# Kernel tuning notes

Hardware: AMD Instinct MI355X
Metric: run time of the kernel (lower is better)

The kernel has to match this reference:

```python
import jax, jax.numpy as jnp
import numpy as np

DIN = 1024
DOUT = 1024


def setup_inputs() -> dict:
    key = jax.random.key(0)
    kx, kq, kk, kv = jax.random.split(key, 4)
    B, T = 4, 2048
    x = jax.random.normal(kx, (B, T, DIN), dtype=jnp.float32)
    # nn.Linear weights are (dout, din); init like PyTorch default scale
    s = 1.0 / np.sqrt(DIN)
    Wq = jax.random.uniform(kq, (DOUT, DIN), minval=-s, maxval=s, dtype=jnp.float32)
    Wk = jax.random.uniform(kk, (DOUT, DIN), minval=-s, maxval=s, dtype=jnp.float32)
    Wv = jax.random.uniform(kv, (DOUT, DIN), minval=-s, maxval=s, dtype=jnp.float32)
    return {"x": x, "Wq": Wq, "Wk": Wk, "Wv": Wv}


def reference(x, Wq, Wk, Wv):
    B, T, _ = x.shape
    q = jnp.einsum('btd,ed->bte', x, Wq)
    k = jnp.einsum('btd,ed->bte', x, Wk)
    v = jnp.einsum('btd,ed->bte', x, Wv)
    attn = jnp.einsum('bqe,bke->bqk', q, k)  # [B, T, T]
    # Faithful to source: masked_fill result is discarded, so the causal mask
    # is a MULTIPLICATIVE tril of ones (upper triangle logits become 0, not -inf).
    mask = jnp.tril(jnp.ones((T, T), dtype=attn.dtype))
    attn = attn * mask
    # Faithful to source: scale by sqrt(last dim of attn) = sqrt(T), not sqrt(d).
    attn = jax.nn.softmax(attn / jnp.sqrt(jnp.asarray(T, attn.dtype)), axis=-1)
    return jnp.einsum('bqk,bke->bqe', attn, v)
```

## Files before the change

kernel.cpp:

```cpp
#include <hip/hip_runtime.h>
#include <stdint.h>

#define BB 4
#define TT 2048
#define DD 1024
#define NX (BB*TT*DD)
#define NW (DD*DD)
#define SCALE 0.022097086912079608f

typedef short v8s __attribute__((ext_vector_type(8)));
typedef float v4f __attribute__((ext_vector_type(4)));

typedef const void __attribute__((address_space(1))) *as1_cvp;
typedef void __attribute__((address_space(3))) *as3_vp;

__device__ __forceinline__ short f2bf(float f) {
    union { float f; uint32_t u; } x; x.f = f;
    uint32_t r = x.u + 0x7fffu + ((x.u >> 16) & 1u);
    return (short)(r >> 16);
}
__device__ __forceinline__ float bf2f(short s) {
    union { uint32_t u; float f; } x; x.u = ((uint32_t)(uint16_t)s) << 16;
    return x.f;
}

__device__ __forceinline__ void gl_lds16(const short* g, const short* lds_wave_base) {
    __builtin_amdgcn_global_load_lds(
        (as1_cvp)(uintptr_t)(const void*)g,
        (as3_vp)(uint32_t)(uintptr_t)(const void*)lds_wave_base,
        16, 0, 0);
}

__device__ __forceinline__ void stage_tile(const short* __restrict__ gsrc, int lda,
                                           short* lds, int tid) {
    int wave = tid >> 6;
    #pragma unroll
    for (int is = 0; is < 4; is++) {
        int t = is * 256 + tid;
        int r = t >> 3, c = t & 7;
        int cg = c ^ (r & 7);
        const short* g = gsrc + (size_t)r * lda + cg * 8;
        const short* l = lds + is * 2048 + wave * 512;
        gl_lds16(g, l);
    }
}
__device__ __forceinline__ void stage_tile64(const short* __restrict__ gsrc, int lda,
                                             short* lds, int tid) {
    int wave = tid >> 6;
    #pragma unroll
    for (int is = 0; is < 2; is++) {
        int t = is * 256 + tid;
        int r = t >> 3, c = t & 7;
        int cg = c ^ (r & 7);
        const short* g = gsrc + (size_t)r * lda + cg * 8;
        const short* l = lds + is * 2048 + wave * 512;
        gl_lds16(g, l);
    }
}
__device__ __forceinline__ v8s frag_read(const short* lds, int row, int cg) {
    return *(const v8s*)(lds + row * 64 + ((cg ^ (row & 7)) << 3));
}

__device__ __forceinline__ void stageA128(const short* __restrict__ g, short* lds, int tid) {
    int wave = tid >> 6;
    #pragma unroll
    for (int s = 0; s < 2; s++) {
        int t = s * 512 + tid;
        int r = t >> 3, c = t & 7;
        int cg = c ^ (r & 7);
        gl_lds16(g + (size_t)r * 1024 + cg * 8, lds + s * 4096 + wave * 512);
    }
}
__device__ __forceinline__ void stageBpart(const short* __restrict__ g, short* lds,
                                           int tid, int p) {
    int wave = tid >> 6;
    #pragma unroll
    for (int s = 0; s < 2; s++) {
        int t = s * 512 + tid;
        int r = t >> 3, c = t & 7;
        int cg = c ^ (r & 7);
        int grow = ((r >> 5) << 6) + p * 32 + (r & 31);
        gl_lds16(g + (size_t)grow * 1024 + cg * 8, lds + s * 4096 + wave * 512);
    }
}

#define COMPUTE_TILE64(Ac, Bc)                                                      \
    _Pragma("unroll")                                                               \
    for (int kk = 0; kk < 2; kk++) {                                                \
        v8s af[2], bf[4];                                                           \
        _Pragma("unroll")                                                           \
        for (int i = 0; i < 2; i++) af[i] = frag_read(Ac, wm + i*16 + lr, kk*4 + lq); \
        _Pragma("unroll")                                                           \
        for (int j = 0; j < 4; j++) bf[j] = frag_read(Bc, wn + j*16 + lr, kk*4 + lq); \
        _Pragma("unroll")                                                           \
        for (int i = 0; i < 2; i++)                                                 \
            _Pragma("unroll")                                                       \
            for (int j = 0; j < 4; j++)                                             \
                acc[i][j] = __builtin_amdgcn_mfma_f32_16x16x32_bf16(af[i], bf[j], acc[i][j], 0, 0, 0); \
    }

__global__ void k_convert(const float* __restrict__ x, const float* __restrict__ Wq,
                          const float* __restrict__ Wk, const float* __restrict__ Wv,
                          short* __restrict__ dst, float* __restrict__ rowsum) {
    int i = blockIdx.x * 256 + threadIdx.x;
    if (i < BB * TT) rowsum[i] = (float)((15 - ((i & 2047) >> 7)) * 128);
    size_t base = (size_t)i * 4;
    const float* src; size_t off;
    if (base < NX)               { src = x;  off = base; }
    else if (base < NX + NW)     { src = Wq; off = base - NX; }
    else if (base < NX + 2*(size_t)NW) { src = Wk; off = base - NX - NW; }
    else                         { src = Wv; off = base - NX - 2*(size_t)NW; }
    float4 f = *(const float4*)(src + off);
    short4 h; h.x = f2bf(f.x); h.y = f2bf(f.y); h.z = f2bf(f.z); h.w = f2bf(f.w);
    *(short4*)(dst + base) = h;
}

__global__ __launch_bounds__(512, 2) void k_qkv(const short* __restrict__ xb,
                                                const short* __restrict__ wb,
                                                short* __restrict__ q,
                                                short* __restrict__ k,
                                                short* __restrict__ vt) {
    int h = blockIdx.x;
    int w = (h & 7) * 96 + (h >> 3);
    int which = w >> 8, rem = w & 255, ntile = rem >> 6, mtile = rem & 63;
    int m0 = mtile * 128, n0 = ntile * 256;
    const short* Ag = xb + (size_t)m0 * 1024;
    const short* Bg = wb + (size_t)which * NW + (size_t)n0 * 1024;
    __shared__ __align__(16) short SH[49152];
    int tid = threadIdx.x, lane = tid & 63, wave = tid >> 6;
    int wm = wave >> 2, wn = wave & 3;
    int lr = lane & 15, lq = lane >> 4;
    int arow = wm * 64 + lr;
    int brow = wn * 32 + lr;
    v4f acc[4][4];
    #pragma unroll
    for (int i = 0; i < 4; i++)
        #pragma unroll
        for (int j = 0; j < 4; j++) acc[i][j] = (v4f){0.f, 0.f, 0.f, 0.f};

    stageA128 (Ag, SH,         tid);
    stageBpart(Bg, SH + 8192,  tid, 0);
    stageBpart(Bg, SH + 16384, tid, 1);

    #pragma unroll
    for (int t = 0; t < 16; ++t) {
        short* S  = SH + (t & 1) * 24576;
        short* Sn = SH + ((t + 1) & 1) * 24576;
        const short* Agn = Ag + (t + 1) * 64;
        const short* Bgn = Bg + (t + 1) * 64;
        asm volatile("s_waitcnt vmcnt(2)" ::: "memory");
        __builtin_amdgcn_s_barrier();
        v8s af[4][2], bf[2][2];
        #pragma unroll
        for (int i = 0; i < 4; i++)
            #pragma unroll
            for (int kk = 0; kk < 2; kk++) af[i][kk] = frag_read(S, arow + i * 16, kk * 4 + lq);
        #pragma unroll
        for (int jj = 0; jj < 2; jj++)
            #pragma unroll
            for (int kk = 0; kk < 2; kk++) bf[jj][kk] = frag_read(S + 8192, brow + jj * 16, kk * 4 + lq);
        if (t < 15) {
            stageA128 (Agn, Sn,        tid);
            stageBpart(Bgn, Sn + 8192, tid, 0);
        }
        __builtin_amdgcn_s_setprio(1);
        #pragma unroll
        for (int kk = 0; kk < 2; kk++)
            #pragma unroll
            for (int i = 0; i < 4; i++)
                #pragma unroll
                for (int jj = 0; jj < 2; jj++)
                    acc[i][jj] = __builtin_amdgcn_mfma_f32_16x16x32_bf16(af[i][kk], bf[jj][kk], acc[i][jj], 0, 0, 0);
        __builtin_amdgcn_s_setprio(0);
        if (t < 15) { asm volatile("s_waitcnt vmcnt(4)" ::: "memory"); }
        else        { asm volatile("s_waitcnt vmcnt(0)" ::: "memory"); }
        __builtin_amdgcn_s_barrier();
        v8s bg2[2][2];
        #pragma unroll
        for (int jj = 0; jj < 2; jj++)
            #pragma unroll
            for (int kk = 0; kk < 2; kk++) bg2[jj][kk] = frag_read(S + 16384, brow + jj * 16, kk * 4 + lq);
        if (t < 15) stageBpart(Bgn, Sn + 16384, tid, 1);
        __builtin_amdgcn_s_setprio(1);
        #pragma unroll
        for (int kk = 0; kk < 2; kk++)
            #pragma unroll
            for (int i = 0; i < 4; i++)
                #pragma unroll
                for (int jj = 0; jj < 2; jj++)
                    acc[i][2 + jj] = __builtin_amdgcn_mfma_f32_16x16x32_bf16(af[i][kk], bg2[jj][kk], acc[i][2 + jj], 0, 0, 0);
        __builtin_amdgcn_s_setprio(0);
    }

    if (which == 2) {
        #pragma unroll
        for (int a = 0; a < 4; a++)
            #pragma unroll
            for (int b = 0; b < 4; b++)
                #pragma unroll
                for (int r = 0; r < 4; r++) {
                    int row = m0 + wm * 64 + a * 16 + lq * 4 + r;
                    int col = n0 + wn * 64 + b * 16 + lr;
                    int bb = row >> 11, tt2 = row & 2047;
                    vt[((size_t)bb << 21) + ((size_t)col << 11) + tt2] = f2bf(acc[a][b][r]);
                }
    } else {
        short* outp = (which == 0) ? q : k;
        #pragma unroll
        for (int a = 0; a < 4; a++)
            #pragma unroll
            for (int b = 0; b < 4; b++)
                #pragma unroll
                for (int r = 0; r < 4; r++) {
                    int row = m0 + wm * 64 + a * 16 + lq * 4 + r;
                    int col = n0 + wn * 64 + b * 16 + lr;
                    outp[(size_t)row * 1024 + col] = f2bf(acc[a][b][r]);
                }
    }
}

__global__ void k_ts1(const short* __restrict__ vt, float* __restrict__ TSpart) {
    int g = blockIdx.x * 256 + threadIdx.x;
    int b = g >> 14, jt = (g >> 10) & 15, e = g & 1023;
    const short* row = vt + ((size_t)b << 21) + ((size_t)e << 11) + jt * 128;
    float s = 0.f;
    #pragma unroll
    for (int c = 0; c < 16; c++) {
        uint4 u = *(const uint4*)(row + c * 8);
        const short* hp = (const short*)&u;
        #pragma unroll
        for (int z = 0; z < 8; z++) s += bf2f(hp[z]);
    }
    TSpart[g] = s;
}
__global__ void k_ts2(const float* __restrict__ TSpart, float* __restrict__ TS) {
    int g = blockIdx.x * 256 + threadIdx.x;
    int b = g >> 10, e = g & 1023;
    float acc = 0.f;
    TS[(size_t)(b * 17 + 16) * 1024 + e] = 0.f;
    for (int jt = 15; jt >= 0; jt--) {
        acc += TSpart[(size_t)(b * 16 + jt) * 1024 + e];
        TS[(size_t)(b * 17 + jt) * 1024 + e] = acc;
    }
}

__global__ __launch_bounds__(256, 3) void k_pk(const short* __restrict__ qm,
                                               const short* __restrict__ km,
                                               short* __restrict__ P,
                                               float* __restrict__ rowsum) {
    int flip = 271 - blockIdx.x, b = blockIdx.z;
    int half = flip & 1, pidx = flip >> 1;
    int qt = 0;
    while ((qt + 1) * (qt + 2) / 2 <= pidx) qt++;
    int kt = pidx - qt * (qt + 1) / 2;
    int r0 = qt * 128 + half * 64;
    const short* Ag = qm + ((size_t)b * 2048 + r0) * 1024;
    const short* Bg = km + ((size_t)b * 2048 + (size_t)kt * 128) * 1024;
    __shared__ __align__(16) short SH[24576];
    int tid = threadIdx.x, lane = tid & 63, wave = tid >> 6;
    int wm = (wave >> 1) * 32, wn = (wave & 1) * 64;
    int lr = lane & 15, lq = lane >> 4;
    v4f acc[2][4];
    for (int i = 0; i < 2; i++) for (int j = 0; j < 4; j++) acc[i][j] = (v4f){0.f,0.f,0.f,0.f};

    stage_tile64(Ag, 1024, SH, tid);
    stage_tile(Bg, 1024, SH + 8192, tid);
    #pragma unroll
    for (int it = 0; it < 16; ++it) {
        __syncthreads();
        short* Ac = SH + (it & 1) * 4096;
        short* Bc = SH + 8192 + (it & 1) * 8192;
        if (it + 1 < 16) {
            stage_tile64(Ag + (it + 1) * 64, 1024, SH + ((it + 1) & 1) * 4096, tid);
            stage_tile  (Bg + (it + 1) * 64, 1024, SH + 8192 + ((it + 1) & 1) * 8192, tid);
        }
        COMPUTE_TILE64(Ac, Bc);
    }
    short* Pb = P + ((size_t)b << 22);
    float rs[2][4];
    for (int i = 0; i < 2; i++) for (int r = 0; r < 4; r++) rs[i][r] = 0.f;
    #pragma unroll
    for (int i = 0; i < 2; i++)
        #pragma unroll
        for (int j = 0; j < 4; j++)
            #pragma unroll
            for (int r = 0; r < 4; r++) {
                int qi = r0 + wm + i*16 + lq*4 + r;
                int kj = kt * 128 + wn + j*16 + lr;
                float p = (kj <= qi) ? __expf(acc[i][j][r] * SCALE) : 1.0f;
                Pb[(size_t)qi * 2048 + kj] = f2bf(p);
                rs[i][r] += p;
            }
    #pragma unroll
    for (int m = 1; m < 16; m <<= 1)
        #pragma unroll
        for (int i = 0; i < 2; i++)
            #pragma unroll
            for (int r = 0; r < 4; r++) rs[i][r] += __shfl_xor(rs[i][r], m);
    if (lr == 0)
        #pragma unroll
        for (int i = 0; i < 2; i++)
            #pragma unroll
            for (int r = 0; r < 4; r++)
                atomicAdd(&rowsum[b * 2048 + r0 + wm + i*16 + lq*4 + r], rs[i][r]);
}

__global__ __launch_bounds__(256, 3) void k_pv(const short* __restrict__ P,
                                               const short* __restrict__ vt,
                                               const float* __restrict__ rowsum,
                                               const float* __restrict__ TS,
                                               float* __restrict__ out) {
    int et = blockIdx.x, p = blockIdx.y >> 1, half = blockIdx.y & 1, b = blockIdx.z;
    const short* Bg = vt + ((size_t)b << 21) + (size_t)et * 128 * 2048;
    __shared__ __align__(16) short SH[24576];
    int tid = threadIdx.x, lane = tid & 63, wave = tid >> 6;
    int wm = (wave >> 1) * 32, wn = (wave & 1) * 64;
    int lr = lane & 15, lq = lane >> 4;

    #pragma unroll
    for (int ph = 0; ph < 2; ph++) {
        int qt = ph ? p : 15 - p;
        int r0 = qt * 128 + half * 64;
        int iters = 2 * (qt + 1);
        const short* Ag = P + ((size_t)b << 22) + (size_t)r0 * 2048;
        v4f acc[2][4];
        for (int i = 0; i < 2; i++) for (int j = 0; j < 4; j++) acc[i][j] = (v4f){0.f,0.f,0.f,0.f};

        stage_tile64(Ag, 2048, SH, tid);
        stage_tile(Bg, 2048, SH + 8192, tid);
        for (int it = 0; it < iters; it += 2) {
            __syncthreads();
            if (it + 1 < iters) {
                stage_tile64(Ag + (it + 1) * 64, 2048, SH + 4096, tid);
                stage_tile  (Bg + (it + 1) * 64, 2048, SH + 8192 + 8192, tid);
            }
            COMPUTE_TILE64(SH, SH + 8192);
            __syncthreads();
            if (it + 2 < iters) {
                stage_tile64(Ag + (it + 2) * 64, 2048, SH, tid);
                stage_tile  (Bg + (it + 2) * 64, 2048, SH + 8192, tid);
            }
            COMPUTE_TILE64(SH + 4096, SH + 8192 + 8192);
        }
        const float* tsrow = TS + (size_t)(b * 17 + qt + 1) * 1024;
        #pragma unroll
        for (int i = 0; i < 2; i++)
            #pragma unroll
            for (int j = 0; j < 4; j++)
                #pragma unroll
                for (int r = 0; r < 4; r++) {
                    int row = r0 + wm + i*16 + lq*4 + r;
                    int col = et * 128 + wn + j*16 + lr;
                    float o = (acc[i][j][r] + tsrow[col]) / rowsum[b * 2048 + row];
                    out[((size_t)(b * 2048 + row) << 10) + col] = o;
                }
        __syncthreads();
    }
}

extern "C" void kernel_launch(void* const* d_in, const int* in_sizes, int n_in,
                              void* d_out, int out_size, void* d_ws, size_t ws_size,
                              hipStream_t stream) {
    const float* x  = (const float*)d_in[0];
    const float* Wq = (const float*)d_in[1];
    const float* Wk = (const float*)d_in[2];
    const float* Wv = (const float*)d_in[3];
    float* out = (float*)d_out;
    char* ws = (char*)d_ws;

    short* xb     = (short*)(ws + 0);
    short* wb     = (short*)(ws + 16777216);
    short* q      = (short*)(ws + 23068672);
    short* k      = (short*)(ws + 39845888);
    short* vt     = (short*)(ws + 56623104);
    short* P      = (short*)(ws + 73400320);
    float* rowsum = (float*)(ws + 106954752);
    float* TSpart = (float*)(ws + 106987520);
    float* TS     = (float*)(ws + 107249664);

    k_convert<<<11264, 256, 0, stream>>>(x, Wq, Wk, Wv, xb, rowsum);
    k_qkv<<<dim3(768, 1, 1), 512, 0, stream>>>(xb, wb, q, k, vt);
    k_ts1<<<256, 256, 0, stream>>>(vt, TSpart);
    k_ts2<<<16, 256, 0, stream>>>(TSpart, TS);
    k_pk<<<dim3(272, 1, 4), 256, 0, stream>>>(q, k, P, rowsum);
    k_pv<<<dim3(8, 16, 4), 256, 0, stream>>>(P, vt, rowsum, TS, out);
}
```

Before: 224.8 us.

## Fuse Q/K/V projections into one block sharing the staged x tile

The QKV GEMM is restructured so each 1024-thread block computes the Q, K and V outputs for one 128x256 tile. It stages the x (A) tile once and reuses it against the three weight matrices, where previously separate blocks each reloaded it. The K-loop start is rotated per m-tile to spread global reads, and a new three-buffer B pipeline with its own waitcnt/barrier schedule is added. In exchange there are fewer blocks (256) with more registers (three accumulator sets) and 128KB of LDS, so occupancy and load balance may suffer.

```diff
diff --git a/kernel.cpp b/kernel.cpp
--- a/kernel.cpp
+++ b/kernel.cpp
@@ -61,26 +61,16 @@
     return *(const v8s*)(lds + row * 64 + ((cg ^ (row & 7)) << 3));
 }
 
-__device__ __forceinline__ void stageA128(const short* __restrict__ g, short* lds, int tid) {
-    int wave = tid >> 6;
+__device__ __forceinline__ void stA(const short* __restrict__ g, short* lds, int tid) {
+    int r = tid >> 3, c = tid & 7, cg = c ^ (r & 7);
+    gl_lds16(g + (size_t)r * 1024 + cg * 8, lds + (tid >> 6) * 512);
+}
+__device__ __forceinline__ void stB(const short* __restrict__ g, short* lds, int tid) {
     #pragma unroll
     for (int s = 0; s < 2; s++) {
-        int t = s * 512 + tid;
-        int r = t >> 3, c = t & 7;
-        int cg = c ^ (r & 7);
-        gl_lds16(g + (size_t)r * 1024 + cg * 8, lds + s * 4096 + wave * 512);
-    }
-}
-__device__ __forceinline__ void stageBpart(const short* __restrict__ g, short* lds,
-                                           int tid, int p) {
-    int wave = tid >> 6;
-    #pragma unroll
-    for (int s = 0; s < 2; s++) {
-        int t = s * 512 + tid;
-        int r = t >> 3, c = t & 7;
-        int cg = c ^ (r & 7);
-        int grow = ((r >> 5) << 6) + p * 32 + (r & 31);
-        gl_lds16(g + (size_t)grow * 1024 + cg * 8, lds + s * 4096 + wave * 512);
+        int t = s * 1024 + tid;
+        int r = t >> 3, c = t & 7, cg = c ^ (r & 7);
+        gl_lds16(g + (size_t)r * 1024 + cg * 8, lds + s * 8192 + (tid >> 6) * 512);
     }
 }
 
@@ -115,108 +105,129 @@
     *(short4*)(dst + base) = h;
 }
 
-__global__ __launch_bounds__(512, 2) void k_qkv(const short* __restrict__ xb,
-                                                const short* __restrict__ wb,
-                                                short* __restrict__ q,
-                                                short* __restrict__ k,
-                                                short* __restrict__ vt) {
+__global__ __launch_bounds__(1024, 4) void k_qkv(const short* __restrict__ xb,
+                                                 const short* __restrict__ wb,
+                                                 short* __restrict__ q,
+                                                 short* __restrict__ k,
+                                                 short* __restrict__ vt) {
     int h = blockIdx.x;
-    int w = (h & 7) * 96 + (h >> 3);
-    int which = w >> 8, rem = w & 255, ntile = rem >> 6, mtile = rem & 63;
+    int w = (h & 7) * 32 + (h >> 3);
+    int ntile = w >> 6, mtile = w & 63;
     int m0 = mtile * 128, n0 = ntile * 256;
+    int rot = mtile & 15;
     const short* Ag = xb + (size_t)m0 * 1024;
-    const short* Bg = wb + (size_t)which * NW + (size_t)n0 * 1024;
-    __shared__ __align__(16) short SH[49152];
+    const short* Bq = wb + (size_t)n0 * 1024;
+    const short* Bk = wb + (size_t)NW + (size_t)n0 * 1024;
+    const short* Bv = wb + 2 * (size_t)NW + (size_t)n0 * 1024;
+    __shared__ __align__(16) short SH[65536];
+    short* SA0 = SH;
+    short* SA1 = SH + 8192;
+    short* SB0 = SH + 16384;
+    short* SB1 = SH + 32768;
+    short* SB2 = SH + 49152;
     int tid = threadIdx.x, lane = tid & 63, wave = tid >> 6;
-    int wm = wave >> 2, wn = wave & 3;
+    int wm2 = wave >> 3, wn8 = wave & 7;
     int lr = lane & 15, lq = lane >> 4;
-    int arow = wm * 64 + lr;
-    int brow = wn * 32 + lr;
-    v4f acc[4][4];
+    int arow = wm2 * 64 + lr;
+    int brow = wn8 * 32 + lr;
+    v4f aq[4][2], ak[4][2], av[4][2];
     #pragma unroll
     for (int i = 0; i < 4; i++)
         #pragma unroll
-        for (int j = 0; j < 4; j++) acc[i][j] = (v4f){0.f, 0.f, 0.f, 0.f};
-
-    stageA128 (Ag, SH,         tid);
-    stageBpart(Bg, SH + 8192,  tid, 0);
-    stageBpart(Bg, SH + 16384, tid, 1);
-
-    #pragma unroll
+        for (int j = 0; j < 2; j++) {
+            aq[i][j] = (v4f){0.f, 0.f, 0.f, 0.f};
+            ak[i][j] = (v4f){0.f, 0.f, 0.f, 0.f};
+            av[i][j] = (v4f){0.f, 0.f, 0.f, 0.f};
+        }
+
+    {
+        int kt0 = rot;
+        stA(Ag + kt0 * 64, SA0, tid);
+        stB(Bq + kt0 * 64, SB0, tid);
+        stB(Bk + kt0 * 64, SB1, tid);
+    }
+    asm volatile("s_waitcnt vmcnt(2)" ::: "memory");
+    __builtin_amdgcn_s_barrier();
+
+    #pragma unroll 2
     for (int t = 0; t < 16; ++t) {
-        short* S  = SH + (t & 1) * 24576;
-        short* Sn = SH + ((t + 1) & 1) * 24576;
-        const short* Agn = Ag + (t + 1) * 64;
-        const short* Bgn = Bg + (t + 1) * 64;
-        asm volatile("s_waitcnt vmcnt(2)" ::: "memory");
-        __builtin_amdgcn_s_barrier();
+        short* SA  = (t & 1) ? SA1 : SA0;
+        short* SAn = (t & 1) ? SA0 : SA1;
+        int kt  = (t + rot) & 15;
+        int ktn = (t + 1 + rot) & 15;
         v8s af[4][2], bf[2][2];
         #pragma unroll
         for (int i = 0; i < 4; i++)
             #pragma unroll
-            for (int kk = 0; kk < 2; kk++) af[i][kk] = frag_read(S, arow + i * 16, kk * 4 + lq);
-        #pragma unroll
-        for (int jj = 0; jj < 2; jj++)
-            #pragma unroll
-            for (int kk = 0; kk < 2; kk++) bf[jj][kk] = frag_read(S + 8192, brow + jj * 16, kk * 4 + lq);
-        if (t < 15) {
-            stageA128 (Agn, Sn,        tid);
-            stageBpart(Bgn, Sn + 8192, tid, 0);
-        }
+            for (int kk = 0; kk < 2; kk++) af[i][kk] = frag_read(SA, arow + i * 16, kk * 4 + lq);
+        #pragma unroll
+        for (int j = 0; j < 2; j++)
+            #pragma unroll
+            for (int kk = 0; kk < 2; kk++) bf[j][kk] = frag_read(SB0, brow + j * 16, kk * 4 + lq);
+        stB(Bv + kt * 64, SB2, tid);
+        if (t < 15) stA(Ag + ktn * 64, SAn, tid);
         __builtin_amdgcn_s_setprio(1);
         #pragma unroll
         for (int kk = 0; kk < 2; kk++)
             #pragma unroll
             for (int i = 0; i < 4; i++)
                 #pragma unroll
-                for (int jj = 0; jj < 2; jj++)
-                    acc[i][jj] = __builtin_amdgcn_mfma_f32_16x16x32_bf16(af[i][kk], bf[jj][kk], acc[i][jj], 0, 0, 0);
+                for (int j = 0; j < 2; j++)
+                    aq[i][j] = __builtin_amdgcn_mfma_f32_16x16x32_bf16(af[i][kk], bf[j][kk], aq[i][j], 0, 0, 0);
         __builtin_amdgcn_s_setprio(0);
-        if (t < 15) { asm volatile("s_waitcnt vmcnt(4)" ::: "memory"); }
+        if (t < 15) { asm volatile("s_waitcnt vmcnt(3)" ::: "memory"); }
+        else        { asm volatile("s_waitcnt vmcnt(2)" ::: "memory"); }
+        __builtin_amdgcn_s_barrier();
+        #pragma unroll
+        for (int j = 0; j < 2; j++)
+            #pragma unroll
+            for (int kk = 0; kk < 2; kk++) bf[j][kk] = frag_read(SB1, brow + j * 16, kk * 4 + lq);
+        if (t < 15) stB(Bq + ktn * 64, SB0, tid);
+        __builtin_amdgcn_s_setprio(1);
+        #pragma unroll
+        for (int kk = 0; kk < 2; kk++)
+            #pragma unroll
+            for (int i = 0; i < 4; i++)
+                #pragma unroll
+                for (int j = 0; j < 2; j++)
+                    ak[i][j] = __builtin_amdgcn_mfma_f32_16x16x32_bf16(af[i][kk], bf[j][kk], ak[i][j], 0, 0, 0);
+        __builtin_amdgcn_s_setprio(0);
+        if (t < 15) { asm volatile("s_waitcnt vmcnt(3)" ::: "memory"); }
         else        { asm volatile("s_waitcnt vmcnt(0)" ::: "memory"); }
         __builtin_amdgcn_s_barrier();
-        v8s bg2[2][2];
-        #pragma unroll
-        for (int jj = 0; jj < 2; jj++)
-            #pragma unroll
-            for (int kk = 0; kk < 2; kk++) bg2[jj][kk] = frag_read(S + 16384, brow + jj * 16, kk * 4 + lq);
-        if (t < 15) stageBpart(Bgn, Sn + 16384, tid, 1);
+        #pragma unroll
+        for (int j = 0; j < 2; j++)
+            #pragma unroll
+            for (int kk = 0; kk < 2; kk++) bf[j][kk] = frag_read(SB2, brow + j * 16, kk * 4 + lq);
+        if (t < 15) stB(Bk + ktn * 64, SB1, tid);
         __builtin_amdgcn_s_setprio(1);
         #pragma unroll
         for (int kk = 0; kk < 2; kk++)
             #pragma unroll
             for (int i = 0; i < 4; i++)
                 #pragma unroll
-                for (int jj = 0; jj < 2; jj++)
-                    acc[i][2 + jj] = __builtin_amdgcn_mfma_f32_16x16x32_bf16(af[i][kk], bg2[jj][kk], acc[i][2 + jj], 0, 0, 0);
+                for (int j = 0; j < 2; j++)
+                    av[i][j] = __builtin_amdgcn_mfma_f32_16x16x32_bf16(af[i][kk], bf[j][kk], av[i][j], 0, 0, 0);
         __builtin_amdgcn_s_setprio(0);
-    }
-
-    if (which == 2) {
-        #pragma unroll
-        for (int a = 0; a < 4; a++)
-            #pragma unroll
-            for (int b = 0; b < 4; b++)
-                #pragma unroll
-                for (int r = 0; r < 4; r++) {
-                    int row = m0 + wm * 64 + a * 16 + lq * 4 + r;
-                    int col = n0 + wn * 64 + b * 16 + lr;
-                    int bb = row >> 11, tt2 = row & 2047;
-                    vt[((size_t)bb << 21) + ((size_t)col << 11) + tt2] = f2bf(acc[a][b][r]);
-                }
-    } else {
-        short* outp = (which == 0) ? q : k;
-        #pragma unroll
-        for (int a = 0; a < 4; a++)
-            #pragma unroll
-            for (int b = 0; b < 4; b++)
-                #pragma unroll
-                for (int r = 0; r < 4; r++) {
-                    int row = m0 + wm * 64 + a * 16 + lq * 4 + r;
-                    int col = n0 + wn * 64 + b * 16 + lr;
-                    outp[(size_t)row * 1024 + col] = f2bf(acc[a][b][r]);
-                }
-    }
+        if (t < 15) {
+            asm volatile("s_waitcnt vmcnt(2)" ::: "memory");
+            __builtin_amdgcn_s_barrier();
+        }
+    }
+
+    #pragma unroll
+    for (int i = 0; i < 4; i++)
+        #pragma unroll
+        for (int j = 0; j < 2; j++)
+            #pragma unroll
+            for (int r = 0; r < 4; r++) {
+                int row = m0 + wm2 * 64 + i * 16 + lq * 4 + r;
+                int col = n0 + wn8 * 32 + j * 16 + lr;
+                q[(size_t)row * 1024 + col] = f2bf(aq[i][j][r]);
+                k[(size_t)row * 1024 + col] = f2bf(ak[i][j][r]);
+                int bb = row >> 11, tt2 = row & 2047;
+                vt[((size_t)bb << 21) + ((size_t)col << 11) + tt2] = f2bf(av[i][j][r]);
+            }
 }
 
 __global__ void k_ts1(const short* __restrict__ vt, float* __restrict__ TSpart) {
@@ -379,7 +390,7 @@
     float* TS     = (float*)(ws + 107249664);
 
     k_convert<<<11264, 256, 0, stream>>>(x, Wq, Wk, Wv, xb, rowsum);
-    k_qkv<<<dim3(768, 1, 1), 512, 0, stream>>>(xb, wb, q, k, vt);
+    k_qkv<<<dim3(256, 1, 1), 1024, 0, stream>>>(xb, wb, q, k, vt);
     k_ts1<<<256, 256, 0, stream>>>(vt, TSpart);
     k_ts2<<<16, 256, 0, stream>>>(TSpart, TS);
     k_pk<<<dim3(272, 1, 4), 256, 0, stream>>>(q, k, P, rowsum);
```

Result: slower. 499.0 us (+121.9%).

## Use 128x128 tiles with 8 waves in score and PV kernels

Applied to the files above, without the earlier changes.

The QK^T score kernel and the PV kernel move from 64x128 tiles with 4 waves to full 128x128 tiles with 8 waves per block, each wave owning a 64x32 sub-tile. This halves the number of blocks and doubles the reuse of each staged K/V tile, aiming to cut global-to-LDS traffic. MFMA sections are wrapped in s_setprio raises, and PV now uses single-step double buffering. The trade-off is larger LDS per block, fewer blocks for load balancing across the triangular work, and the loss of the reversed block ordering in the score kernel.

```diff
diff --git a/kernel.cpp b/kernel.cpp
--- a/kernel.cpp
+++ b/kernel.cpp
@@ -31,73 +31,32 @@
         16, 0, 0);
 }
 
-__device__ __forceinline__ void stage_tile(const short* __restrict__ gsrc, int lda,
-                                           short* lds, int tid) {
-    int wave = tid >> 6;
-    #pragma unroll
-    for (int is = 0; is < 4; is++) {
-        int t = is * 256 + tid;
-        int r = t >> 3, c = t & 7;
-        int cg = c ^ (r & 7);
-        const short* g = gsrc + (size_t)r * lda + cg * 8;
-        const short* l = lds + is * 2048 + wave * 512;
-        gl_lds16(g, l);
-    }
-}
-__device__ __forceinline__ void stage_tile64(const short* __restrict__ gsrc, int lda,
-                                             short* lds, int tid) {
-    int wave = tid >> 6;
-    #pragma unroll
-    for (int is = 0; is < 2; is++) {
-        int t = is * 256 + tid;
-        int r = t >> 3, c = t & 7;
-        int cg = c ^ (r & 7);
-        const short* g = gsrc + (size_t)r * lda + cg * 8;
-        const short* l = lds + is * 2048 + wave * 512;
-        gl_lds16(g, l);
-    }
-}
 __device__ __forceinline__ v8s frag_read(const short* lds, int row, int cg) {
     return *(const v8s*)(lds + row * 64 + ((cg ^ (row & 7)) << 3));
 }
 
-__device__ __forceinline__ void stageA128(const short* __restrict__ g, short* lds, int tid) {
-    int wave = tid >> 6;
+__device__ __forceinline__ void stage128_512(const short* __restrict__ g, int lda,
+                                             short* lds, int tid) {
     #pragma unroll
     for (int s = 0; s < 2; s++) {
         int t = s * 512 + tid;
-        int r = t >> 3, c = t & 7;
-        int cg = c ^ (r & 7);
-        gl_lds16(g + (size_t)r * 1024 + cg * 8, lds + s * 4096 + wave * 512);
-    }
+        int r = t >> 3, c = t & 7, cg = c ^ (r & 7);
+        gl_lds16(g + (size_t)r * lda + cg * 8, lds + s * 4096 + (tid >> 6) * 512);
+    }
+}
+__device__ __forceinline__ void stageA128(const short* __restrict__ g, short* lds, int tid) {
+    stage128_512(g, 1024, lds, tid);
 }
 __device__ __forceinline__ void stageBpart(const short* __restrict__ g, short* lds,
                                            int tid, int p) {
-    int wave = tid >> 6;
     #pragma unroll
     for (int s = 0; s < 2; s++) {
         int t = s * 512 + tid;
-        int r = t >> 3, c = t & 7;
-        int cg = c ^ (r & 7);
+        int r = t >> 3, c = t & 7, cg = c ^ (r & 7);
         int grow = ((r >> 5) << 6) + p * 32 + (r & 31);
-        gl_lds16(g + (size_t)grow * 1024 + cg * 8, lds + s * 4096 + wave * 512);
-    }
-}
-
-#define COMPUTE_TILE64(Ac, Bc)                                                      \
-    _Pragma("unroll")                                                               \
-    for (int kk = 0; kk < 2; kk++) {                                                \
-        v8s af[2], bf[4];                                                           \
-        _Pragma("unroll")                                                           \
-        for (int i = 0; i < 2; i++) af[i] = frag_read(Ac, wm + i*16 + lr, kk*4 + lq); \
-        _Pragma("unroll")                                                           \
-        for (int j = 0; j < 4; j++) bf[j] = frag_read(Bc, wn + j*16 + lr, kk*4 + lq); \
-        _Pragma("unroll")                                                           \
-        for (int i = 0; i < 2; i++)                                                 \
-            _Pragma("unroll")                                                       \
-            for (int j = 0; j < 4; j++)                                             \
-                acc[i][j] = __builtin_amdgcn_mfma_f32_16x16x32_bf16(af[i], bf[j], acc[i][j], 0, 0, 0); \
-    }
+        gl_lds16(g + (size_t)grow * 1024 + cg * 8, lds + s * 4096 + (tid >> 6) * 512);
+    }
+}
 
 __global__ void k_convert(const float* __restrict__ x, const float* __restrict__ Wq,
                           const float* __restrict__ Wk, const float* __restrict__ Wv,
@@ -244,49 +203,71 @@
     }
 }
 
-__global__ __launch_bounds__(256, 3) void k_pk(const short* __restrict__ qm,
+__global__ __launch_bounds__(512, 4) void k_pk(const short* __restrict__ qm,
                                                const short* __restrict__ km,
                                                short* __restrict__ P,
                                                float* __restrict__ rowsum) {
-    int flip = 271 - blockIdx.x, b = blockIdx.z;
-    int half = flip & 1, pidx = flip >> 1;
+    int pidx = blockIdx.x, b = blockIdx.z;
     int qt = 0;
     while ((qt + 1) * (qt + 2) / 2 <= pidx) qt++;
     int kt = pidx - qt * (qt + 1) / 2;
-    int r0 = qt * 128 + half * 64;
+    int r0 = qt * 128;
     const short* Ag = qm + ((size_t)b * 2048 + r0) * 1024;
     const short* Bg = km + ((size_t)b * 2048 + (size_t)kt * 128) * 1024;
-    __shared__ __align__(16) short SH[24576];
+    __shared__ __align__(16) short SH[32768];
     int tid = threadIdx.x, lane = tid & 63, wave = tid >> 6;
-    int wm = (wave >> 1) * 32, wn = (wave & 1) * 64;
+    int wm2 = wave >> 2, wn4 = wave & 3;
     int lr = lane & 15, lq = lane >> 4;
-    v4f acc[2][4];
-    for (int i = 0; i < 2; i++) for (int j = 0; j < 4; j++) acc[i][j] = (v4f){0.f,0.f,0.f,0.f};
-
-    stage_tile64(Ag, 1024, SH, tid);
-    stage_tile(Bg, 1024, SH + 8192, tid);
+    v4f acc[4][2];
+    #pragma unroll
+    for (int i = 0; i < 4; i++)
+        #pragma unroll
+        for (int j = 0; j < 2; j++) acc[i][j] = (v4f){0.f, 0.f, 0.f, 0.f};
+
+    stage128_512(Ag, 1024, SH, tid);
+    stage128_512(Bg, 1024, SH + 16384, tid);
     #pragma unroll
     for (int it = 0; it < 16; ++it) {
         __syncthreads();
-        short* Ac = SH + (it & 1) * 4096;
-        short* Bc = SH + 8192 + (it & 1) * 8192;
+        short* Ac = SH + (it & 1) * 8192;
+        short* Bc = SH + 16384 + (it & 1) * 8192;
         if (it + 1 < 16) {
-            stage_tile64(Ag + (it + 1) * 64, 1024, SH + ((it + 1) & 1) * 4096, tid);
-            stage_tile  (Bg + (it + 1) * 64, 1024, SH + 8192 + ((it + 1) & 1) * 8192, tid);
+            stage128_512(Ag + (it + 1) * 64, 1024, SH + ((it + 1) & 1) * 8192, tid);
+            stage128_512(Bg + (it + 1) * 64, 1024, SH + 16384 + ((it + 1) & 1) * 8192, tid);
         }
-        COMPUTE_TILE64(Ac, Bc);
+        v8s af[4][2], bf[2][2];
+        #pragma unroll
+        for (int i = 0; i < 4; i++)
+            #pragma unroll
+            for (int kk = 0; kk < 2; kk++) af[i][kk] = frag_read(Ac, wm2 * 64 + i * 16 + lr, kk * 4 + lq);
+        #pragma unroll
+        for (int j = 0; j < 2; j++)
+            #pragma unroll
+            for (int kk = 0; kk < 2; kk++) bf[j][kk] = frag_read(Bc, wn4 * 32 + j * 16 + lr, kk * 4 + lq);
+        __builtin_amdgcn_s_setprio(1);
+        #pragma unroll
+        for (int kk = 0; kk < 2; kk++)
+            #pragma unroll
+            for (int i = 0; i < 4; i++)
+                #pragma unroll
+                for (int j = 0; j < 2; j++)
+                    acc[i][j] = __builtin_amdgcn_mfma_f32_16x16x32_bf16(af[i][kk], bf[j][kk], acc[i][j], 0, 0, 0);
+        __builtin_amdgcn_s_setprio(0);
     }
     short* Pb = P + ((size_t)b << 22);
-    float rs[2][4];
-    for (int i = 0; i < 2; i++) for (int r = 0; r < 4; r++) rs[i][r] = 0.f;
-    #pragma unroll
-    for (int i = 0; i < 2; i++)
-        #pragma unroll
-        for (int j = 0; j < 4; j++)
+    float rs[4][4];
+    #pragma unroll
+    for (int i = 0; i < 4; i++)
+        #pragma unroll
+        for (int r = 0; r < 4; r++) rs[i][r] = 0.f;
+    #pragma unroll
+    for (int i = 0; i < 4; i++)
+        #pragma unroll
+        for (int j = 0; j < 2; j++)
             #pragma unroll
             for (int r = 0; r < 4; r++) {
-                int qi = r0 + wm + i*16 + lq*4 + r;
-                int kj = kt * 128 + wn + j*16 + lr;
+                int qi = r0 + wm2 * 64 + i * 16 + lq * 4 + r;
+                int kj = kt * 128 + wn4 * 32 + j * 16 + lr;
                 float p = (kj <= qi) ? __expf(acc[i][j][r] * SCALE) : 1.0f;
                 Pb[(size_t)qi * 2048 + kj] = f2bf(p);
                 rs[i][r] += p;
@@ -294,63 +275,79 @@
     #pragma unroll
     for (int m = 1; m < 16; m <<= 1)
         #pragma unroll
-        for (int i = 0; i < 2; i++)
+        for (int i = 0; i < 4; i++)
             #pragma unroll
             for (int r = 0; r < 4; r++) rs[i][r] += __shfl_xor(rs[i][r], m);
     if (lr == 0)
         #pragma unroll
-        for (int i = 0; i < 2; i++)
+        for (int i = 0; i < 4; i++)
             #pragma unroll
             for (int r = 0; r < 4; r++)
-                atomicAdd(&rowsum[b * 2048 + r0 + wm + i*16 + lq*4 + r], rs[i][r]);
-}
-
-__global__ __launch_bounds__(256, 3) void k_pv(const short* __restrict__ P,
+                atomicAdd(&rowsum[b * 2048 + r0 + wm2 * 64 + i * 16 + lq * 4 + r], rs[i][r]);
+}
+
+__global__ __launch_bounds__(512, 4) void k_pv(const short* __restrict__ P,
                                                const short* __restrict__ vt,
                                                const float* __restrict__ rowsum,
                                                const float* __restrict__ TS,
                                                float* __restrict__ out) {
-    int et = blockIdx.x, p = blockIdx.y >> 1, half = blockIdx.y & 1, b = blockIdx.z;
+    int et = blockIdx.x, p = blockIdx.y, b = blockIdx.z;
     const short* Bg = vt + ((size_t)b << 21) + (size_t)et * 128 * 2048;
-    __shared__ __align__(16) short SH[24576];
+    __shared__ __align__(16) short SH[32768];
     int tid = threadIdx.x, lane = tid & 63, wave = tid >> 6;
-    int wm = (wave >> 1) * 32, wn = (wave & 1) * 64;
+    int wm2 = wave >> 2, wn4 = wave & 3;
     int lr = lane & 15, lq = lane >> 4;
 
     #pragma unroll
     for (int ph = 0; ph < 2; ph++) {
         int qt = ph ? p : 15 - p;
-        int r0 = qt * 128 + half * 64;
+        int r0 = qt * 128;
         int iters = 2 * (qt + 1);
         const short* Ag = P + ((size_t)b << 22) + (size_t)r0 * 2048;
-        v4f acc[2][4];
-        for (int i = 0; i < 2; i++) for (int j = 0; j < 4; j++) acc[i][j] = (v4f){0.f,0.f,0.f,0.f};
-
-        stage_tile64(Ag, 2048, SH, tid);
-        stage_tile(Bg, 2048, SH + 8192, tid);
-        for (int it = 0; it < iters; it += 2) {
+        v4f acc[4][2];
+        #pragma unroll
+        for (int i = 0; i < 4; i++)
+            #pragma unroll
+            for (int j = 0; j < 2; j++) acc[i][j] = (v4f){0.f, 0.f, 0.f, 0.f};
+
+        stage128_512(Ag, 2048, SH, tid);
+        stage128_512(Bg, 2048, SH + 16384, tid);
+        for (int it = 0; it < iters; ++it) {
             __syncthreads();
+            short* Ac = SH + (it & 1) * 8192;
+            short* Bc = SH + 16384 + (it & 1) * 8192;
             if (it + 1 < iters) {
-                stage_tile64(Ag + (it + 1) * 64, 2048, SH + 4096, tid);
-                stage_tile  (Bg + (it + 1) * 64, 2048, SH + 8192 + 8192, tid);
+                stage128_512(Ag + (it + 1) * 64, 2048, SH + ((it + 1) & 1) * 8192, tid);
+                stage128_512(Bg + (it + 1) * 64, 2048, SH + 16384 + ((it + 1) & 1) * 8192, tid);
             }
-            COMPUTE_TILE64(SH, SH + 8192);
-            __syncthreads();
-            if (it + 2 < iters) {
-                stage_tile64(Ag + (it + 2) * 64, 2048, SH, tid);
-                stage_tile  (Bg + (it + 2) * 64, 2048, SH + 8192, tid);
-            }
-            COMPUTE_TILE64(SH + 4096, SH + 8192 + 8192);
+            v8s af[4][2], bf[2][2];
+            #pragma unroll
+            for (int i = 0; i < 4; i++)
+                #pragma unroll
+                for (int kk = 0; kk < 2; kk++) af[i][kk] = frag_read(Ac, wm2 * 64 + i * 16 + lr, kk * 4 + lq);
+            #pragma unroll
+            for (int j = 0; j < 2; j++)
+                #pragma unroll
+                for (int kk = 0; kk < 2; kk++) bf[j][kk] = frag_read(Bc, wn4 * 32 + j * 16 + lr, kk * 4 + lq);
+            __builtin_amdgcn_s_setprio(1);
+            #pragma unroll
+            for (int kk = 0; kk < 2; kk++)
+                #pragma unroll
+                for (int i = 0; i < 4; i++)
+                    #pragma unroll
+                    for (int j = 0; j < 2; j++)
+                        acc[i][j] = __builtin_amdgcn_mfma_f32_16x16x32_bf16(af[i][kk], bf[j][kk], acc[i][j], 0, 0, 0);
+            __builtin_amdgcn_s_setprio(0);
         }
         const float* tsrow = TS + (size_t)(b * 17 + qt + 1) * 1024;
         #pragma unroll
-        for (int i = 0; i < 2; i++)
-            #pragma unroll
-            for (int j = 0; j < 4; j++)
+        for (int i = 0; i < 4; i++)
+            #pragma unroll
+            for (int j = 0; j < 2; j++)
                 #pragma unroll
                 for (int r = 0; r < 4; r++) {
-                    int row = r0 + wm + i*16 + lq*4 + r;
-                    int col = et * 128 + wn + j*16 + lr;
+                    int row = r0 + wm2 * 64 + i * 16 + lq * 4 + r;
+                    int col = et * 128 + wn4 * 32 + j * 16 + lr;
                     float o = (acc[i][j][r] + tsrow[col]) / rowsum[b * 2048 + row];
                     out[((size_t)(b * 2048 + row) << 10) + col] = o;
                 }
@@ -382,6 +379,6 @@
     k_qkv<<<dim3(768, 1, 1), 512, 0, stream>>>(xb, wb, q, k, vt);
     k_ts1<<<256, 256, 0, stream>>>(vt, TSpart);
     k_ts2<<<16, 256, 0, stream>>>(TSpart, TS);
-    k_pk<<<dim3(272, 1, 4), 256, 0, stream>>>(q, k, P, rowsum);
-    k_pv<<<dim3(8, 16, 4), 256, 0, stream>>>(P, vt, rowsum, TS, out);
-}
+    k_pk<<<dim3(136, 1, 4), 512, 0, stream>>>(q, k, P, rowsum);
+    k_pv<<<dim3(8, 8, 4), 512, 0, stream>>>(P, vt, rowsum, TS, out);
+}
```

Result: slower. 237.3 us (+5.6%).

## Triple-buffer QKV GEMM LDS pipeline and rotate K-start per block

Applied to the files above, without the earlier changes.

The QKV projection GEMM goes from a double-buffered LDS pipeline to a three-stage ring buffer. LDS grows from 96KB to 144KB per block, and loads are issued two to three K-steps ahead with the vmcnt waits retuned to match. Each block also starts its K loop at a rotated offset, which spreads concurrent global reads across different address regions. The larger LDS footprint may cut occupancy below the two blocks per CU requested in launch bounds, and the hand-counted waits are easy to get wrong.

```diff
diff --git a/kernel.cpp b/kernel.cpp
--- a/kernel.cpp
+++ b/kernel.cpp
@@ -30,6 +30,12 @@
         (as3_vp)(uint32_t)(uintptr_t)(const void*)lds_wave_base,
         16, 0, 0);
 }
+
+__device__ __forceinline__ v8s frag_read(const short* lds, int row, int cg) {
+    return *(const v8s*)(lds + row * 64 + ((cg ^ (row & 7)) << 3));
+}
+
+#define WAITV(N) asm volatile("s_waitcnt vmcnt(" #N ")" ::: "memory")
 
 __device__ __forceinline__ void stage_tile(const short* __restrict__ gsrc, int lda,
                                            short* lds, int tid) {
@@ -57,30 +63,23 @@
         gl_lds16(g, l);
     }
 }
-__device__ __forceinline__ v8s frag_read(const short* lds, int row, int cg) {
-    return *(const v8s*)(lds + row * 64 + ((cg ^ (row & 7)) << 3));
-}
 
 __device__ __forceinline__ void stageA128(const short* __restrict__ g, short* lds, int tid) {
-    int wave = tid >> 6;
     #pragma unroll
     for (int s = 0; s < 2; s++) {
         int t = s * 512 + tid;
-        int r = t >> 3, c = t & 7;
-        int cg = c ^ (r & 7);
-        gl_lds16(g + (size_t)r * 1024 + cg * 8, lds + s * 4096 + wave * 512);
+        int r = t >> 3, c = t & 7, cg = c ^ (r & 7);
+        gl_lds16(g + (size_t)r * 1024 + cg * 8, lds + s * 4096 + (tid >> 6) * 512);
     }
 }
 __device__ __forceinline__ void stageBpart(const short* __restrict__ g, short* lds,
                                            int tid, int p) {
-    int wave = tid >> 6;
     #pragma unroll
     for (int s = 0; s < 2; s++) {
         int t = s * 512 + tid;
-        int r = t >> 3, c = t & 7;
-        int cg = c ^ (r & 7);
+        int r = t >> 3, c = t & 7, cg = c ^ (r & 7);
         int grow = ((r >> 5) << 6) + p * 32 + (r & 31);
-        gl_lds16(g + (size_t)grow * 1024 + cg * 8, lds + s * 4096 + wave * 512);
+        gl_lds16(g + (size_t)grow * 1024 + cg * 8, lds + s * 4096 + (tid >> 6) * 512);
     }
 }
 
@@ -124,9 +123,10 @@
     int w = (h & 7) * 96 + (h >> 3);
     int which = w >> 8, rem = w & 255, ntile = rem >> 6, mtile = rem & 63;
     int m0 = mtile * 128, n0 = ntile * 256;
+    int rot = (mtile + 4 * ntile + 5 * which) & 15;
     const short* Ag = xb + (size_t)m0 * 1024;
     const short* Bg = wb + (size_t)which * NW + (size_t)n0 * 1024;
-    __shared__ __align__(16) short SH[49152];
+    __shared__ __align__(16) short SH[73728];
     int tid = threadIdx.x, lane = tid & 63, wave = tid >> 6;
     int wm = wave >> 2, wn = wave & 3;
     int lr = lane & 15, lq = lane >> 4;
@@ -138,17 +138,21 @@
         #pragma unroll
         for (int j = 0; j < 4; j++) acc[i][j] = (v4f){0.f, 0.f, 0.f, 0.f};
 
-    stageA128 (Ag, SH,         tid);
-    stageBpart(Bg, SH + 8192,  tid, 0);
-    stageBpart(Bg, SH + 16384, tid, 1);
+    #pragma unroll
+    for (int t = 0; t < 3; ++t) {
+        int kt = (t + rot) & 15;
+        short* S = SH + t * 24576;
+        stageA128 (Ag + kt * 64, S,         tid);
+        stageBpart(Bg + kt * 64, S + 8192,  tid, 0);
+        if (t < 2) stageBpart(Bg + kt * 64, S + 16384, tid, 1);
+    }
 
     #pragma unroll
     for (int t = 0; t < 16; ++t) {
-        short* S  = SH + (t & 1) * 24576;
-        short* Sn = SH + ((t + 1) & 1) * 24576;
-        const short* Agn = Ag + (t + 1) * 64;
-        const short* Bgn = Bg + (t + 1) * 64;
-        asm volatile("s_waitcnt vmcnt(2)" ::: "memory");
+        short* S = SH + (t % 3) * 24576;
+        if (t <= 13)      { WAITV(12); }
+        else if (t == 14) { WAITV(8);  }
+        else              { WAITV(2);  }
         __builtin_amdgcn_s_barrier();
         v8s af[4][2], bf[2][2];
         #pragma unroll
@@ -159,9 +163,9 @@
         for (int jj = 0; jj < 2; jj++)
             #pragma unroll
             for (int kk = 0; kk < 2; kk++) bf[jj][kk] = frag_read(S + 8192, brow + jj * 16, kk * 4 + lq);
-        if (t < 15) {
-            stageA128 (Agn, Sn,        tid);
-            stageBpart(Bgn, Sn + 8192, tid, 0);
+        if (t + 2 <= 15) {
+            int kt2 = (t + 2 + rot) & 15;
+            stageBpart(Bg + kt2 * 64, SH + ((t + 2) % 3) * 24576 + 16384, tid, 1);
         }
         __builtin_amdgcn_s_setprio(1);
         #pragma unroll
@@ -172,15 +176,21 @@
                 for (int jj = 0; jj < 2; jj++)
                     acc[i][jj] = __builtin_amdgcn_mfma_f32_16x16x32_bf16(af[i][kk], bf[jj][kk], acc[i][jj], 0, 0, 0);
         __builtin_amdgcn_s_setprio(0);
-        if (t < 15) { asm volatile("s_waitcnt vmcnt(4)" ::: "memory"); }
-        else        { asm volatile("s_waitcnt vmcnt(0)" ::: "memory"); }
+        if (t <= 13)      { WAITV(12); }
+        else if (t == 14) { WAITV(6);  }
+        else              { WAITV(0);  }
         __builtin_amdgcn_s_barrier();
         v8s bg2[2][2];
         #pragma unroll
         for (int jj = 0; jj < 2; jj++)
             #pragma unroll
             for (int kk = 0; kk < 2; kk++) bg2[jj][kk] = frag_read(S + 16384, brow + jj * 16, kk * 4 + lq);
-        if (t < 15) stageBpart(Bgn, Sn + 16384, tid, 1);
+        if (t + 3 <= 15) {
+            int kt3 = (t + 3 + rot) & 15;
+            short* Sn = SH + (t % 3) * 24576;
+            stageA128 (Ag + kt3 * 64, Sn,        tid);
+            stageBpart(Bg + kt3 * 64, Sn + 8192, tid, 0);
+        }
         __builtin_amdgcn_s_setprio(1);
         #pragma unroll
         for (int kk = 0; kk < 2; kk++)
```

After: 229.7 us. 2.2% more time.
